# Performance work log

Measured on AMD Instinct MI355X. Metric: run time of the kernel, lower is better.

Reference implementation:

```python
import jax, jax.numpy as jnp
import numpy as np

B, T, D_IN = 32, 32, 128
N_SLOTS, M_LEN = 512, 64
NUM_SHIFT, NUM_READ, NUM_WRITE = 3, 4, 1
CTRL_DIM = 256
READ_HEAD_LEN = 3 + M_LEN + NUM_SHIFT            # k, beta, g, s, gamma
WRITE_HEAD_LEN = READ_HEAD_LEN + 2 * M_LEN       # + erase, add vectors
INSTR_DIM = NUM_READ * READ_HEAD_LEN + NUM_WRITE * WRITE_HEAD_LEN


def setup_inputs() -> dict:
    key = jax.random.key(0)
    ks = jax.random.split(key, 4)
    def glorot(k, shape):
        lim = np.sqrt(6.0 / (shape[0] + shape[1])).astype(np.float32)
        return jax.random.uniform(k, shape, jnp.float32, -lim, lim)
    return {
        "x": jax.random.normal(ks[0], (B, T, D_IN), jnp.float32),
        "Wc": glorot(ks[1], (D_IN + NUM_READ * M_LEN, CTRL_DIM)),
        "bc": jnp.zeros((CTRL_DIM,), jnp.float32),
        "heads_kernel": glorot(ks[2], (CTRL_DIM, INSTR_DIM)),
        "heads_bias": jnp.zeros((INSTR_DIM,), jnp.float32),
    }


def _parse_heads(h):
    # h: (B, H, 3 + M + S) -> k, beta, g, s, gamma per _get_weight_vector
    k = h[..., :M_LEN]
    b = jnp.exp(h[..., M_LEN])
    g = jax.nn.sigmoid(h[..., M_LEN + 1])
    s = jax.nn.softmax(h[..., M_LEN + 2:M_LEN + 2 + NUM_SHIFT], axis=-1)
    t = jax.nn.softplus(h[..., M_LEN + 2 + NUM_SHIFT]) + 1.0
    return k, b, g, s, t


def _address(Mem, w_prev, k, b, g, s, t):
    # Mem:(B,N,M) k:(B,H,M) w_prev:(B,H,N) b,g,t:(B,H) s:(B,H,S)
    eps = 1e-8
    Mn = jnp.linalg.norm(Mem, axis=-1)                       # (B,N)
    kn = jnp.linalg.norm(k, axis=-1)                         # (B,H)
    sim = jnp.einsum('bhm,bnm->bhn', k, Mem) / (kn[..., None] * Mn[:, None, :] + eps)
    wc = jax.nn.softmax(b[..., None] * sim, axis=-1)         # content
    wg = g[..., None] * wc + (1.0 - g[..., None]) * w_prev   # gate
    half = NUM_SHIFT // 2                                    # circular shift conv
    wsh = sum(s[..., i:i + 1] * jnp.roll(wg, i - half, axis=-1) for i in range(NUM_SHIFT))
    wt = wsh ** t[..., None]                                 # sharpen
    return wt / (jnp.sum(wt, axis=-1, keepdims=True) + eps)


def _ntm_forward(x, Wc, bc, heads_kernel, heads_bias):
    def step(carry, x_t):
        r, rw, ww, Mem = carry
        # dense controller on [x_t, old read vectors]
        ctrl_in = jnp.concatenate([x_t, r.reshape(B, -1)], axis=-1)
        h = jnp.tanh(ctrl_in @ Wc + bc)                      # controller_out == instr
        instr = h @ heads_kernel + heads_bias                # (B, INSTR_DIM)
        rh = instr[:, :NUM_READ * READ_HEAD_LEN].reshape(B, NUM_READ, READ_HEAD_LEN)
        wh = instr[:, NUM_READ * READ_HEAD_LEN:].reshape(B, NUM_WRITE, WRITE_HEAD_LEN)
        rw_n = _address(Mem, rw, *_parse_heads(rh))
        ww_n = _address(Mem, ww, *_parse_heads(wh[..., :READ_HEAD_LEN]))
        e = wh[..., READ_HEAD_LEN:READ_HEAD_LEN + M_LEN]     # raw erase (no sigmoid, as in source)
        a = wh[..., READ_HEAD_LEN + M_LEN:]                  # raw add
        # erase all heads, then add all heads (source loops erase first)
        Mem = Mem * jnp.prod(1.0 - ww_n[..., :, None] * e[..., None, :], axis=1)
        Mem = Mem + jnp.einsum('bwn,bwm->bnm', ww_n, a)
        r_n = jnp.einsum('bnm,brn->brm', Mem, rw_n)          # read
        return (r_n, rw_n, ww_n, Mem), h

    init = (jnp.zeros((B, NUM_READ, M_LEN), jnp.float32),
            jnp.zeros((B, NUM_READ, N_SLOTS), jnp.float32),
            jnp.zeros((B, NUM_WRITE, N_SLOTS), jnp.float32),
            jnp.zeros((B, N_SLOTS, M_LEN), jnp.float32))
    _, outs = jax.lax.scan(step, init, jnp.swapaxes(x, 0, 1))  # time-major
    return outs[-1]  # return_sequences=False -> last controller output (B, CTRL_DIM)


def reference(x, Wc, bc, heads_kernel, heads_bias):
    return _ntm_forward(x, Wc, bc, heads_kernel, heads_bias)
```

## Files before the change

kernel.cpp:

```cpp
#include <hip/hip_runtime.h>
#include <math.h>

#define BB 32
#define TT 32
#define D_INX 128
#define NSLOT 512
#define MLEN 64
#define NREAD 4
#define NHEAD 5
#define CDIM 256
#define IDIM 478
#define RHL 70
#define NT 512

#define XP_SZ   1048576
#define WCT_OFF XP_SZ
#define HKB_OFF (XP_SZ + 262144)

struct SMem {
    float mem[NSLOT * MLEN];
    float w4[NSLOT * 4];
    float ww[NSLOT];
    float mn[NSLOT];
    float ctrl[256];
    float h[CDIM];
    float instr[480];
    float k[NHEAD * MLEN];
    float e[MLEN];
    float a[MLEN];
    float u[NHEAD * NSLOT];
};

__device__ __forceinline__ float rlane(float v, int l) {
    return __int_as_float(__builtin_amdgcn_readlane(__float_as_int(v), l));
}

__global__ void pack_kernel(const float* __restrict__ Wc, const float* __restrict__ Hk,
                            float* __restrict__ wct, float* __restrict__ hkb)
{
    int idx = blockIdx.x * 256 + threadIdx.x;
    if (idx < 256 * 256) {
        int i = idx >> 8, col = idx & 255;
        wct[((i >> 3) * 256 + col) * 8 + (i & 7)] = Wc[(128 + i) * 256 + col];
    }
    if (idx < 256 * 478) {
        int i = idx / 478, col = idx - i * 478;
        hkb[((i >> 3) * 478 + col) * 8 + (i & 7)] = Hk[i * 478 + col];
    }
}

__global__ __launch_bounds__(256)
void xpart_kernel(const float* __restrict__ x, const float* __restrict__ Wc,
                  const float* __restrict__ bc, float* __restrict__ xp)
{
    __shared__ float xs[D_INX];
    const int bt = blockIdx.x, col = threadIdx.x;
    if (col < D_INX) xs[col] = x[(size_t)bt * D_INX + col];
    __syncthreads();
    float acc = bc[col];
#pragma unroll 8
    for (int k = 0; k < D_INX; ++k) acc += xs[k] * Wc[k * 256 + col];
    xp[(size_t)bt * CDIM + col] = acc;
}

#define P1_CHUNK(cg_) do {                                                      \
    const float4 w0 = wqa[(cg_) * 512];                                         \
    const float4 w1 = wqa[(cg_) * 512 + 1];                                     \
    const int k0 = (cg_) * 8;                                                   \
    float a0 = rlane(creg[(k0 + 0) >> 6], (k0 + 0) & 63);                       \
    float a1 = rlane(creg[(k0 + 1) >> 6], (k0 + 1) & 63);                       \
    float a2 = rlane(creg[(k0 + 2) >> 6], (k0 + 2) & 63);                       \
    float a3 = rlane(creg[(k0 + 3) >> 6], (k0 + 3) & 63);                       \
    float a4 = rlane(creg[(k0 + 4) >> 6], (k0 + 4) & 63);                       \
    float a5 = rlane(creg[(k0 + 5) >> 6], (k0 + 5) & 63);                       \
    float a6 = rlane(creg[(k0 + 6) >> 6], (k0 + 6) & 63);                       \
    float a7 = rlane(creg[(k0 + 7) >> 6], (k0 + 7) & 63);                       \
    accs[(cg_) & 3] += w0.x * a0 + w0.y * a1 + w0.z * a2 + w0.w * a3            \
                     + w1.x * a4 + w1.y * a5 + w1.z * a6 + w1.w * a7;           \
} while (0)

__global__ __launch_bounds__(NT, 2)
void ntm_kernel(const float* __restrict__ xp,
                const float* __restrict__ hb,
                const float* __restrict__ wct,
                const float* __restrict__ hkb,
                float* __restrict__ out)
{
    extern __shared__ float smem_f[];
    SMem* sc = (SMem*)smem_f;

    const int b    = blockIdx.x;
    const int tid  = threadIdx.x;
    const int lane = tid & 63;
    const int wave = tid >> 6;

    const int col   = tid & 255;
    const int halfw = tid >> 8;

    const float hbv = (tid < IDIM) ? hb[tid] : 0.f;

    {
        float4 z4 = make_float4(0.f, 0.f, 0.f, 0.f);
        float4* m4 = (float4*)sc->mem;
        for (int i = tid; i < NSLOT * MLEN / 4; i += NT) m4[i] = z4;
        for (int i = tid; i < NSLOT * 4; i += NT) sc->w4[i] = 0.f;
        if (tid < NSLOT) sc->ww[tid] = 0.f;
        if (tid < 256) sc->ctrl[tid] = 0.f;
    }
    __syncthreads();

    for (int t = 0; t < TT; ++t) {
        {
            const float xpv = xp[(size_t)(b * TT + t) * CDIM + col];

            float creg[4];
            creg[0] = sc->ctrl[lane];
            creg[1] = sc->ctrl[64 + lane];
            creg[2] = sc->ctrl[128 + lane];
            creg[3] = sc->ctrl[192 + lane];

            const float4* wqa = (const float4*)wct + col * 2;
            float accs[4] = {0.f, 0.f, 0.f, 0.f};
            if (halfw == 0) {
#pragma unroll
                for (int cc = 0; cc < 16; ++cc) P1_CHUNK(cc);
            } else {
#pragma unroll
                for (int cc = 0; cc < 16; ++cc) P1_CHUNK(16 + cc);
            }
            float s = (accs[0] + accs[1]) + (accs[2] + accs[3]);
            if (halfw == 1) sc->u[col] = s;
            __syncthreads();
            if (halfw == 0) {
                float z = xpv + s + sc->u[col];
                z = fminf(fmaxf(z, -15.f), 15.f);
                float ex = __expf(2.f * z);
                float hv = (ex - 1.f) / (ex + 1.f);
                sc->h[col] = hv;
                if (t == TT - 1) out[(size_t)b * CDIM + col] = hv;
            }
        }
        if (t == TT - 1) break;
        __syncthreads();

        {
            float hreg[4];
#pragma unroll
            for (int j = 0; j < 4; ++j) hreg[j] = sc->h[64 * j + lane];
            if (tid < IDIM) {
                const float4* wq2a = (const float4*)hkb + tid * 2;
                float accs[4] = {0.f, 0.f, 0.f, 0.f};
#pragma unroll
                for (int c = 0; c < 32; ++c) {
                    const float4 w0 = wq2a[c * 956];
                    const float4 w1 = wq2a[c * 956 + 1];
                    const int k0 = c * 8;
                    float a0 = rlane(hreg[(k0 + 0) >> 6], (k0 + 0) & 63);
                    float a1 = rlane(hreg[(k0 + 1) >> 6], (k0 + 1) & 63);
                    float a2 = rlane(hreg[(k0 + 2) >> 6], (k0 + 2) & 63);
                    float a3 = rlane(hreg[(k0 + 3) >> 6], (k0 + 3) & 63);
                    float a4 = rlane(hreg[(k0 + 4) >> 6], (k0 + 4) & 63);
                    float a5 = rlane(hreg[(k0 + 5) >> 6], (k0 + 5) & 63);
                    float a6 = rlane(hreg[(k0 + 6) >> 6], (k0 + 6) & 63);
                    float a7 = rlane(hreg[(k0 + 7) >> 6], (k0 + 7) & 63);
                    accs[c & 3] += w0.x * a0 + w0.y * a1 + w0.z * a2 + w0.w * a3
                                 + w1.x * a4 + w1.y * a5 + w1.z * a6 + w1.w * a7;
                }
                float acc = hbv + (accs[0] + accs[1]) + (accs[2] + accs[3]);
                sc->instr[tid] = acc;
                if (tid < 350) {
                    int hh = (tid * 937) >> 16;
                    int m = tid - hh * RHL;
                    if (m < MLEN) sc->k[hh * MLEN + m] = acc;
                } else if (tid < 414) {
                    sc->e[tid - 350] = acc;
                } else {
                    sc->a[tid - 414] = acc;
                }
            } else {
                for (int i = tid - IDIM; i < 256; i += NT - IDIM) sc->ctrl[i] = 0.f;
            }
        }
        __syncthreads();

        {
            const int n = tid, nx = n & 15;
            const float4* m4 = (const float4*)sc->mem + n * 16;
            float kreg[5];
#pragma unroll
            for (int h2 = 0; h2 < 5; ++h2) kreg[h2] = sc->k[h2 * MLEN + lane];
            float d0 = 0.f, d1 = 0.f, d2 = 0.f, d3 = 0.f, d4 = 0.f, nsq = 0.f;
#pragma unroll
            for (int j = 0; j < 16; ++j) {
                float4 mv = m4[j ^ nx];
                nsq += mv.x * mv.x + mv.y * mv.y + mv.z * mv.z + mv.w * mv.w;
                d0 += mv.x * rlane(kreg[0], 4*j) + mv.y * rlane(kreg[0], 4*j+1)
                    + mv.z * rlane(kreg[0], 4*j+2) + mv.w * rlane(kreg[0], 4*j+3);
                d1 += mv.x * rlane(kreg[1], 4*j) + mv.y * rlane(kreg[1], 4*j+1)
                    + mv.z * rlane(kreg[1], 4*j+2) + mv.w * rlane(kreg[1], 4*j+3);
                d2 += mv.x * rlane(kreg[2], 4*j) + mv.y * rlane(kreg[2], 4*j+1)
                    + mv.z * rlane(kreg[2], 4*j+2) + mv.w * rlane(kreg[2], 4*j+3);
                d3 += mv.x * rlane(kreg[3], 4*j) + mv.y * rlane(kreg[3], 4*j+1)
                    + mv.z * rlane(kreg[3], 4*j+2) + mv.w * rlane(kreg[3], 4*j+3);
                d4 += mv.x * rlane(kreg[4], 4*j) + mv.y * rlane(kreg[4], 4*j+1)
                    + mv.z * rlane(kreg[4], 4*j+2) + mv.w * rlane(kreg[4], 4*j+3);
            }
            sc->u[n] = d0; sc->u[NSLOT + n] = d1; sc->u[2 * NSLOT + n] = d2;
            sc->u[3 * NSLOT + n] = d3; sc->u[4 * NSLOT + n] = d4;
            sc->mn[n] = sqrtf(nsq);
        }
        __syncthreads();

        if (wave < NHEAD) {
            const int h = wave;
            const float* ins = sc->instr + h * RHL;
            float kv = ins[lane];
            float sq = kv * kv;
#pragma unroll
            for (int off = 32; off; off >>= 1) sq += __shfl_xor(sq, off);
            float kn = sqrtf(sq);
            float beta = __expf(ins[64]);
            float g = 1.f / (1.f + __expf(-ins[65]));
            float v0 = ins[66], v1 = ins[67], v2 = ins[68];
            float mx3 = fmaxf(v0, fmaxf(v1, v2));
            float e0 = __expf(v0 - mx3), e1 = __expf(v1 - mx3), e2 = __expf(v2 - mx3);
            float inv3 = 1.f / (e0 + e1 + e2);
            float s0 = e0 * inv3, s1 = e1 * inv3, s2 = e2 * inv3;
            float tv = ins[69];
            float tp = fmaxf(tv, 0.f) + log1pf(__expf(-fabsf(tv))) + 1.f;

            float uu[8];
#pragma unroll
            for (int j = 0; j < 8; ++j) {
                int slot = j * 64 + lane;
                float d = sc->u[h * NSLOT + slot];
                uu[j] = beta * d / (kn * sc->mn[slot] + 1e-8f);
            }
            float m = uu[0];
#pragma unroll
            for (int j = 1; j < 8; ++j) m = fmaxf(m, uu[j]);
#pragma unroll
            for (int off = 32; off; off >>= 1) m = fmaxf(m, __shfl_xor(m, off));
            float ev[8]; float Z = 0.f;
#pragma unroll
            for (int j = 0; j < 8; ++j) { ev[j] = __expf(uu[j] - m); Z += ev[j]; }
#pragma unroll
            for (int off = 32; off; off >>= 1) Z += __shfl_xor(Z, off);
            float invZ = 1.f / Z;
            float wg[8];
#pragma unroll
            for (int j = 0; j < 8; ++j) {
                int slot = j * 64 + lane;
                float oldw = (h < 4) ? sc->w4[slot * 4 + h] : sc->ww[slot];
                wg[j] = g * ev[j] * invZ + (1.f - g) * oldw;
            }
            int lm = (lane + 63) & 63, lp = (lane + 1) & 63;
            float rm[8], rp[8];
#pragma unroll
            for (int j = 0; j < 8; ++j) {
                float sm = (lane == 63) ? wg[(j + 7) & 7] : wg[j];
                float sp = (lane == 0)  ? wg[(j + 1) & 7] : wg[j];
                rm[j] = __shfl(sm, lm);
                rp[j] = __shfl(sp, lp);
            }
            float wt[8]; float S = 0.f;
#pragma unroll
            for (int j = 0; j < 8; ++j) {
                float wsh = s0 * rp[j] + s1 * wg[j] + s2 * rm[j];
                wt[j] = __builtin_amdgcn_exp2f(tp * __builtin_amdgcn_logf(wsh));
                S += wt[j];
            }
#pragma unroll
            for (int off = 32; off; off >>= 1) S += __shfl_xor(S, off);
            float invS = 1.f / (S + 1e-8f);
#pragma unroll
            for (int j = 0; j < 8; ++j) {
                int slot = j * 64 + lane;
                float wnew = wt[j] * invS;
                if (h < 4) sc->w4[slot * 4 + h] = wnew;
                else       sc->ww[slot] = wnew;
            }
        }
        __syncthreads();

        {
            const int rg = lane >> 4, j = lane & 15, base = wave * 64;
            const float4 ev = ((const float4*)sc->e)[j];
            const float4 av = ((const float4*)sc->a)[j];
            float4* m4 = (float4*)sc->mem;
            float4 ac[4];
#pragma unroll
            for (int hh = 0; hh < 4; ++hh) ac[hh] = make_float4(0.f, 0.f, 0.f, 0.f);
#pragma unroll
            for (int i = 0; i < 16; ++i) {
                const int n = base + 4 * i + rg;
                const int idx = n * 16 + (j ^ (n & 15));
                float4 mv = m4[idx];
                const float wv = sc->ww[n];
                mv.x = mv.x * (1.f - wv * ev.x) + wv * av.x;
                mv.y = mv.y * (1.f - wv * ev.y) + wv * av.y;
                mv.z = mv.z * (1.f - wv * ev.z) + wv * av.z;
                mv.w = mv.w * (1.f - wv * ev.w) + wv * av.w;
                m4[idx] = mv;
                const float4 w4v = ((const float4*)sc->w4)[n];
                ac[0].x += w4v.x * mv.x; ac[0].y += w4v.x * mv.y; ac[0].z += w4v.x * mv.z; ac[0].w += w4v.x * mv.w;
                ac[1].x += w4v.y * mv.x; ac[1].y += w4v.y * mv.y; ac[1].z += w4v.y * mv.z; ac[1].w += w4v.y * mv.w;
                ac[2].x += w4v.z * mv.x; ac[2].y += w4v.z * mv.y; ac[2].z += w4v.z * mv.z; ac[2].w += w4v.z * mv.w;
                ac[3].x += w4v.w * mv.x; ac[3].y += w4v.w * mv.y; ac[3].z += w4v.w * mv.z; ac[3].w += w4v.w * mv.w;
            }
            float* af = (float*)ac;
#pragma unroll
            for (int q = 0; q < 16; ++q) {
                af[q] += __shfl_xor(af[q], 16);
                af[q] += __shfl_xor(af[q], 32);
            }
            if (rg == 0) {
#pragma unroll
                for (int hh = 0; hh < 4; ++hh) {
                    atomicAdd(&sc->ctrl[hh * 64 + 4 * j + 0], ac[hh].x);
                    atomicAdd(&sc->ctrl[hh * 64 + 4 * j + 1], ac[hh].y);
                    atomicAdd(&sc->ctrl[hh * 64 + 4 * j + 2], ac[hh].z);
                    atomicAdd(&sc->ctrl[hh * 64 + 4 * j + 3], ac[hh].w);
                }
            }
        }
        __syncthreads();
    }
}

extern "C" void kernel_launch(void* const* d_in, const int* in_sizes, int n_in,
                              void* d_out, int out_size, void* d_ws, size_t ws_size,
                              hipStream_t stream) {
    const float* x  = (const float*)d_in[0];
    const float* Wc = (const float*)d_in[1];
    const float* bc = (const float*)d_in[2];
    const float* Hk = (const float*)d_in[3];
    const float* hb = (const float*)d_in[4];
    float* out = (float*)d_out;

    float* xp  = (float*)d_ws;
    float* wct = (float*)((char*)d_ws + WCT_OFF);
    float* hkb = (float*)((char*)d_ws + HKB_OFF);

    static_assert(sizeof(SMem) <= 163840, "LDS overflow");
    (void)hipFuncSetAttribute((const void*)ntm_kernel,
                              hipFuncAttributeMaxDynamicSharedMemorySize,
                              (int)sizeof(SMem));

    hipLaunchKernelGGL(pack_kernel, dim3(478), dim3(256), 0, stream, Wc, Hk, wct, hkb);
    hipLaunchKernelGGL(xpart_kernel, dim3(BB * TT), dim3(256), 0, stream, x, Wc, bc, xp);
    hipLaunchKernelGGL(ntm_kernel, dim3(BB), dim3(NT), sizeof(SMem), stream,
                       xp, hb, wct, hkb, out);
}
```

Measured before the change: 772.4 us.

## Compute key-memory similarity with split-bf16 MFMA instead of readlane FMAs

Replaces the per-thread scalar dot products of memory rows against the five head keys, which used readlane broadcasts, with 16x16x32 bf16 MFMA instructions. Precision is emulated by splitting each fp32 operand into bf16 hi and lo parts and issuing three MFMAs (hi*hi, hi*lo, lo*hi). Row norms are still computed in fp32 with a cross-lane reduction. This cuts VALU and readlane work on a per-timestep critical path, at the cost of conversion overhead, a small loss of precision, and MFMA tiles that are mostly padding since only 5 of 16 key columns are used.

```diff
diff --git a/kernel.cpp b/kernel.cpp
--- a/kernel.cpp
+++ b/kernel.cpp
@@ -16,6 +16,9 @@
 #define XP_SZ   1048576
 #define WCT_OFF XP_SZ
 #define HKB_OFF (XP_SZ + 262144)
+
+typedef short bf8 __attribute__((ext_vector_type(8)));
+typedef float f32x4 __attribute__((ext_vector_type(4)));
 
 struct SMem {
     float mem[NSLOT * MLEN];
@@ -33,6 +36,24 @@
 
 __device__ __forceinline__ float rlane(float v, int l) {
     return __int_as_float(__builtin_amdgcn_readlane(__float_as_int(v), l));
+}
+
+__device__ __forceinline__ void cvt_hi_lo(const float* a, bf8* hi, bf8* lo) {
+    union { unsigned u[4]; bf8 v; } H, L;
+#pragma unroll
+    for (int p = 0; p < 4; ++p) {
+        unsigned hu;
+        asm("v_cvt_pk_bf16_f32 %0, %1, %2" : "=v"(hu) : "v"(a[2 * p]), "v"(a[2 * p + 1]));
+        H.u[p] = hu;
+        float h0 = __uint_as_float(hu << 16);
+        float h1 = __uint_as_float(hu & 0xffff0000u);
+        float l0 = a[2 * p] - h0;
+        float l1 = a[2 * p + 1] - h1;
+        unsigned lu;
+        asm("v_cvt_pk_bf16_f32 %0, %1, %2" : "=v"(lu) : "v"(l0), "v"(l1));
+        L.u[p] = lu;
+    }
+    *hi = H.v; *lo = L.v;
 }
 
 __global__ void pack_kernel(const float* __restrict__ Wc, const float* __restrict__ Hk,
@@ -184,30 +205,58 @@
         __syncthreads();
 
         {
-            const int n = tid, nx = n & 15;
-            const float4* m4 = (const float4*)sc->mem + n * 16;
-            float kreg[5];
-#pragma unroll
-            for (int h2 = 0; h2 < 5; ++h2) kreg[h2] = sc->k[h2 * MLEN + lane];
-            float d0 = 0.f, d1 = 0.f, d2 = 0.f, d3 = 0.f, d4 = 0.f, nsq = 0.f;
-#pragma unroll
-            for (int j = 0; j < 16; ++j) {
-                float4 mv = m4[j ^ nx];
-                nsq += mv.x * mv.x + mv.y * mv.y + mv.z * mv.z + mv.w * mv.w;
-                d0 += mv.x * rlane(kreg[0], 4*j) + mv.y * rlane(kreg[0], 4*j+1)
-                    + mv.z * rlane(kreg[0], 4*j+2) + mv.w * rlane(kreg[0], 4*j+3);
-                d1 += mv.x * rlane(kreg[1], 4*j) + mv.y * rlane(kreg[1], 4*j+1)
-                    + mv.z * rlane(kreg[1], 4*j+2) + mv.w * rlane(kreg[1], 4*j+3);
-                d2 += mv.x * rlane(kreg[2], 4*j) + mv.y * rlane(kreg[2], 4*j+1)
-                    + mv.z * rlane(kreg[2], 4*j+2) + mv.w * rlane(kreg[2], 4*j+3);
-                d3 += mv.x * rlane(kreg[3], 4*j) + mv.y * rlane(kreg[3], 4*j+1)
-                    + mv.z * rlane(kreg[3], 4*j+2) + mv.w * rlane(kreg[3], 4*j+3);
-                d4 += mv.x * rlane(kreg[4], 4*j) + mv.y * rlane(kreg[4], 4*j+1)
-                    + mv.z * rlane(kreg[4], 4*j+2) + mv.w * rlane(kreg[4], 4*j+3);
-            }
-            sc->u[n] = d0; sc->u[NSLOT + n] = d1; sc->u[2 * NSLOT + n] = d2;
-            sc->u[3 * NSLOT + n] = d3; sc->u[4 * NSLOT + n] = d4;
-            sc->mn[n] = sqrtf(nsq);
+            const int q   = lane >> 4;
+            const int r15 = lane & 15;
+
+            bf8 bhi[2], blo[2];
+#pragma unroll
+            for (int kc = 0; kc < 2; ++kc) {
+                float kb[8];
+                if (r15 < NHEAD) {
+                    const float4* k4 = (const float4*)(sc->k + r15 * MLEN + kc * 32 + q * 8);
+                    float4 kv0 = k4[0], kv1 = k4[1];
+                    kb[0] = kv0.x; kb[1] = kv0.y; kb[2] = kv0.z; kb[3] = kv0.w;
+                    kb[4] = kv1.x; kb[5] = kv1.y; kb[6] = kv1.z; kb[7] = kv1.w;
+                } else {
+#pragma unroll
+                    for (int i = 0; i < 8; ++i) kb[i] = 0.f;
+                }
+                cvt_hi_lo(kb, &bhi[kc], &blo[kc]);
+            }
+
+#pragma unroll
+            for (int tt = 0; tt < 4; ++tt) {
+                const int tbase = wave * 64 + tt * 16;
+                const int n = tbase + r15;
+                const int nx = n & 15;
+                const float4* m4 = (const float4*)sc->mem + n * 16;
+                f32x4 acc = {0.f, 0.f, 0.f, 0.f};
+                float nsq = 0.f;
+#pragma unroll
+                for (int kc = 0; kc < 2; ++kc) {
+                    const int j0 = kc * 8 + q * 2;
+                    float4 av0 = m4[j0 ^ nx];
+                    float4 av1 = m4[(j0 + 1) ^ nx];
+                    float aa[8];
+                    aa[0] = av0.x; aa[1] = av0.y; aa[2] = av0.z; aa[3] = av0.w;
+                    aa[4] = av1.x; aa[5] = av1.y; aa[6] = av1.z; aa[7] = av1.w;
+#pragma unroll
+                    for (int i = 0; i < 8; ++i) nsq += aa[i] * aa[i];
+                    bf8 ahi, alo;
+                    cvt_hi_lo(aa, &ahi, &alo);
+                    acc = __builtin_amdgcn_mfma_f32_16x16x32_bf16(ahi, bhi[kc], acc, 0, 0, 0);
+                    acc = __builtin_amdgcn_mfma_f32_16x16x32_bf16(ahi, blo[kc], acc, 0, 0, 0);
+                    acc = __builtin_amdgcn_mfma_f32_16x16x32_bf16(alo, bhi[kc], acc, 0, 0, 0);
+                }
+                nsq += __shfl_xor(nsq, 16);
+                nsq += __shfl_xor(nsq, 32);
+                if (q == 0) sc->mn[n] = sqrtf(nsq);
+                if (r15 < NHEAD) {
+                    float4 st;
+                    st.x = acc[0]; st.y = acc[1]; st.z = acc[2]; st.w = acc[3];
+                    *(float4*)&sc->u[r15 * NSLOT + tbase + q * 4] = st;
+                }
+            }
         }
         __syncthreads();
 
```

After: 744.5 us. -3.6%, faster.
